# Kernel optimization log

Measured on AMD Instinct MI355X. Metric: run time of the kernel, lower is better.

Reference implementation:

```python
import jax, jax.numpy as jnp
import numpy as np

N, L, K = 2048, 256, 16

def setup_inputs() -> dict:
    rng = np.random.default_rng(0)
    # per level: wavelet index = l (distinct across levels), plus K-1 random distinct rest indices
    sel = np.zeros((L, K), dtype=np.int64)
    wav = np.arange(L, dtype=np.int64)
    all_idx = np.arange(N)
    for l in range(L):
        others = rng.choice(np.delete(all_idx, l), size=K - 1, replace=False)
        sel[l] = np.sort(np.concatenate([[l], others]))
    key = jax.random.key(0)
    k1, k2 = jax.random.split(key)
    M = jax.random.normal(k1, (N, N), dtype=jnp.float32)
    A = 0.5 * (M + M.T)  # symmetric matrix, as MMF expects
    O_all = jax.random.normal(k2, (L, K, K), dtype=jnp.float32) / np.float32(K) ** 0.5
    return {"A": A, "O_all": O_all, "sel_idx": jnp.asarray(sel), "wav_idx": jnp.asarray(wav)}


def reference(A, O_all, sel_idx, wav_idx):
    # Torch builds a dense NxN U = eye with O scattered into the KxK block at
    # sel_idx x sel_idx, then A <- U A U^T and right <- U @ right.
    # Equivalent efficient form: only the K selected rows/cols change.
    n = A.shape[0]

    def step(carry, xs):
        A, right = carry
        O, idx = xs  # O: (K,K), idx: (K,)
        A = A.at[idx].set(O @ A[idx])              # U @ A   : rewrite K rows
        A = A.at[:, idx].set(A[:, idx] @ O.T)      # ... @ U^T: rewrite K cols
        right = right.at[idx].set(O @ right[idx])  # right <- U @ right
        return (A, right), None

    right0 = jnp.eye(n, dtype=A.dtype)
    (A_f, right), _ = jax.lax.scan(step, (A, right0), (O_all, sel_idx))

    # final_active_index: 1 everywhere except wavelet indices
    active = jnp.ones((n,), dtype=A.dtype).at[wav_idx].set(0.0)
    # left_index = eye - diag(diag(outer)) + outer  -> diag all ones, off-diag = a_i*a_j
    left = jnp.outer(active, active)
    left = left.at[jnp.diag_indices(n)].set(1.0)
    D = A_f * left
    A_rec = right.T @ D @ right
    return (A_rec, right, D)
```

## Files before the change

kernel.cpp:

```cpp
#include <hip/hip_runtime.h>

#define N 2048
#define LEV 256
#define KS 16

typedef __attribute__((ext_vector_type(8))) short bfx8;
typedef __attribute__((ext_vector_type(4))) float fx4;
typedef unsigned short u16;
typedef unsigned int u32;

static const size_t NN = (size_t)N * N;

__device__ inline u16 bf16_rne(float f) {
    u32 u = __builtin_bit_cast(u32, f);
    u32 r = (u + 0x7FFFu + ((u >> 16) & 1u)) >> 16;
    return (u16)r;
}
__device__ inline float bf16_f(u16 h) {
    u32 u = ((u32)h) << 16;
    return __builtin_bit_cast(float, u);
}

#define GLDS16(gp, lp) __builtin_amdgcn_global_load_lds( \
    (const __attribute__((address_space(1))) void*)(uintptr_t)(gp), \
    (__attribute__((address_space(3))) void*)(u32)(uintptr_t)(lp), 16, 0, 0)

__device__ inline float qadd(float x) {
#if __has_builtin(__builtin_amdgcn_mov_dpp)
    int a = __builtin_amdgcn_mov_dpp(__builtin_bit_cast(int, x), 0xB1, 0xF, 0xF, true);
    float y = x + __builtin_bit_cast(float, a);
    int b = __builtin_amdgcn_mov_dpp(__builtin_bit_cast(int, y), 0x4E, 0xF, 0xF, true);
    return y + __builtin_bit_cast(float, b);
#else
    float y = x + __shfl_xor(x, 1);
    return y + __shfl_xor(y, 2);
#endif
}

__global__ __launch_bounds__(64)
void front_k(const float* __restrict__ O_all, const int* __restrict__ sel,
             u16* __restrict__ rth,
             const float* __restrict__ A, u16* __restrict__ a2h) {
    __shared__ float x[2048];
    const int lane = threadIdx.x;

    if (blockIdx.x >= 2048) {
        u16* a2l = a2h + NN;
        size_t p = (((size_t)blockIdx.x - 2048) * 64 + lane) * 8;
        float4 v0 = *(const float4*)(A + p);
        float4 v1 = *(const float4*)(A + p + 4);
        float vv[8] = {v0.x, v0.y, v0.z, v0.w, v1.x, v1.y, v1.z, v1.w};
        bfx8 hs, ls;
        #pragma unroll
        for (int i = 0; i < 8; ++i) {
            u16 h = bf16_rne(vv[i]);
            hs[i] = (short)h;
            ls[i] = (short)bf16_rne(vv[i] - bf16_f(h));
        }
        *(bfx8*)(a2h + p) = hs;
        *(bfx8*)(a2l + p) = ls;
        return;
    }

    const int i    = lane >> 2;
    const int kg   = lane & 3;
    const int col  = blockIdx.x;

    const float4 z = make_float4(0.f, 0.f, 0.f, 0.f);
    #pragma unroll
    for (int q = 0; q < 8; ++q) *(float4*)&x[q * 256 + lane * 4] = z;
    if (lane == 0) x[col] = 1.0f;

    const float* obase = O_all + i * KS + kg * 4;
    const int*   gbase = sel + kg * 4;

#define CMP(f, g, wv) { \
    float p = f.x * x[g.x] + f.y * x[g.y] + f.z * x[g.z] + f.w * x[g.w]; \
    p = qadd(p); \
    if (kg == 0) x[wv] = p; }

    float4 f0 = *(const float4*)(obase);
    int4   g0 = *(const int4*)(gbase);
    int    w0 = sel[i];
    float4 f1 = *(const float4*)(obase + 256);
    int4   g1 = *(const int4*)(gbase + KS);
    int    w1 = sel[KS + i];

    for (int l = 0; l < LEV; l += 2) {
        float4 f2, f3; int4 g2, g3; int w2, w3;
        if (l + 2 < LEV) {
            f2 = *(const float4*)(obase + (size_t)(l + 2) * 256);
            g2 = *(const int4*)(gbase + (l + 2) * KS);
            w2 = sel[(l + 2) * KS + i];
            f3 = *(const float4*)(obase + (size_t)(l + 3) * 256);
            g3 = *(const int4*)(gbase + (l + 3) * KS);
            w3 = sel[(l + 3) * KS + i];
        } else { f2 = f0; g2 = g0; w2 = w0; f3 = f1; g3 = g1; w3 = w1; }

        CMP(f0, g0, w0)
        CMP(f1, g1, w1)
        f0 = f2; g0 = g2; w0 = w2;
        f1 = f3; g1 = g3; w1 = w3;
    }
#undef CMP

    u16* rtl = rth + NN;
    #pragma unroll
    for (int q = 0; q < 8; ++q) {
        float4 v = *(const float4*)&x[q * 256 + lane * 4];
        float vv[4] = {v.x, v.y, v.z, v.w};
        u16 hh[4], ll[4];
        #pragma unroll
        for (int e = 0; e < 4; ++e) {
            hh[e] = bf16_rne(vv[e]);
            ll[e] = bf16_rne(vv[e] - bf16_f(hh[e]));
        }
        const size_t po = (size_t)col * N + q * 256 + lane * 4;
        *(ushort4*)(rth + po) = make_ushort4(hh[0], hh[1], hh[2], hh[3]);
        *(ushort4*)(rtl + po) = make_ushort4(ll[0], ll[1], ll[2], ll[3]);
    }
}

__global__ __launch_bounds__(256)
void split_rt_k(const u16* __restrict__ rth, u16* __restrict__ r2h,
                float* __restrict__ Rrm) {
    __shared__ float t[64][65];
    const u16* rtl = rth + NN;
    u16* r2l = r2h + NN;
    const int r0 = (blockIdx.x >> 5) * 64, c0 = (blockIdx.x & 31) * 64;
    #pragma unroll
    for (int i = 0; i < 16; ++i) {
        int q = i * 256 + threadIdx.x;
        int rr = q >> 6, cc = q & 63;
        const size_t po = (size_t)(r0 + rr) * N + c0 + cc;
        t[rr][cc] = bf16_f(rth[po]) + bf16_f(rtl[po]);
    }
    __syncthreads();
    #pragma unroll
    for (int i = 0; i < 16; ++i) {
        int q = i * 256 + threadIdx.x;
        int rr = q >> 6, cc = q & 63;
        float w = t[cc][rr];
        u16 h2 = bf16_rne(w);
        size_t pt = (size_t)(c0 + rr) * N + r0 + cc;
        r2h[pt] = h2;
        r2l[pt] = bf16_rne(w - bf16_f(h2));
        Rrm[pt] = w;
    }
}

__global__ __launch_bounds__(256)
void unsplit_k(const u16* __restrict__ hi, float* __restrict__ dst) {
    const u16* lo = hi + NN;
    size_t p = ((size_t)blockIdx.x * 256 + threadIdx.x) * 8;
    bfx8 hs = *(const bfx8*)(hi + p);
    bfx8 ls = *(const bfx8*)(lo + p);
    float4 o0, o1;
    o0.x = bf16_f((u16)hs[0]) + bf16_f((u16)ls[0]);
    o0.y = bf16_f((u16)hs[1]) + bf16_f((u16)ls[1]);
    o0.z = bf16_f((u16)hs[2]) + bf16_f((u16)ls[2]);
    o0.w = bf16_f((u16)hs[3]) + bf16_f((u16)ls[3]);
    o1.x = bf16_f((u16)hs[4]) + bf16_f((u16)ls[4]);
    o1.y = bf16_f((u16)hs[5]) + bf16_f((u16)ls[5]);
    o1.z = bf16_f((u16)hs[6]) + bf16_f((u16)ls[6]);
    o1.w = bf16_f((u16)hs[7]) + bf16_f((u16)ls[7]);
    *(float4*)(dst + p)     = o0;
    *(float4*)(dst + p + 4) = o1;
}

template<int MASKED, int OMODE>
__global__ __launch_bounds__(256)
void gemm_bf3(const u16* __restrict__ Xp, const u16* __restrict__ Yp,
              float* __restrict__ Cf, u16* __restrict__ Cs,
              const int* __restrict__ wav, int Lw) {
    __shared__ __align__(16) u16 sm[24576];
    __shared__ float rowf[128], colf[64];

    const int tid = threadIdx.x;
    const int xcd = blockIdx.x & 7, idx = blockIdx.x >> 3;
    const int sup = 4 * xcd + (idx >> 4);
    const int wi4 = idx & 15;
    const int by = (sup >> 3) * 4 + (wi4 >> 2);
    const int bx = (sup & 7) * 4 + (wi4 & 3);
    const int i0 = by * 128, j0 = bx * 64;
    const int lane = tid & 63, w = tid >> 6;
    const int wm = (w >> 1) * 64, wn = (w & 1) * 32;
    const int fr = lane & 15;

    if (MASKED) {
        if (tid < 128) rowf[tid] = 1.0f;
        if (tid >= 128 && tid < 192) colf[tid - 128] = 1.0f;
        __syncthreads();
        for (int t = tid; t < Lw; t += 256) {
            int wv = wav[t];
            int dr = wv - i0; if (0 <= dr && dr < 128) rowf[dr] = 0.0f;
            int dc = wv - j0; if (0 <= dc && dc < 64)  colf[dc] = 0.0f;
        }
    }

    fx4 acc[4][2];
    #pragma unroll
    for (int m = 0; m < 4; ++m)
        #pragma unroll
        for (int n = 0; n < 2; ++n)
            acc[m][n] = (fx4)0.0f;

    const u16* Xh = Xp; const u16* Xl = Xp + NN;
    const u16* Yh = Yp; const u16* Yl = Yp + NN;

    const int rl   = lane >> 3;
    const int gcol = ((lane & 7) ^ rl) << 3;
    const int wq   = w * 1024;

    #define STAGE(kt) { \
        const int k0s = (kt) * 64; \
        char* lb0 = (char*)sm + wq; \
        _Pragma("unroll") \
        for (int q = 0; q < 4; ++q) { \
            const int row = q * 32 + w * 8 + rl; \
            const size_t xo = (size_t)(i0 + row) * N + k0s + gcol; \
            GLDS16(Xh + xo, lb0 + q * 4096); \
            GLDS16(Xl + xo, lb0 + 16384 + q * 4096); \
        } \
        _Pragma("unroll") \
        for (int q = 0; q < 2; ++q) { \
            const int row = q * 32 + w * 8 + rl; \
            const size_t yo = (size_t)(j0 + row) * N + k0s + gcol; \
            GLDS16(Yh + yo, lb0 + 32768 + q * 4096); \
            GLDS16(Yl + yo, lb0 + 40960 + q * 4096); \
        } }

    const int kq  = (lane >> 4) << 4;
    const int frx = (fr & 7) << 4;

    #define COMPUTE() { \
        const char* base = (const char*)sm; \
        _Pragma("unroll") \
        for (int s = 0; s < 2; ++s) { \
            const int cb = s * 64 + kq; \
            bfx8 ah[4], al[4]; \
            _Pragma("unroll") \
            for (int m = 0; m < 4; ++m) { \
                const int off = (wm + m * 16 + fr) * 128 + (cb ^ frx); \
                ah[m] = *(const bfx8*)(base + off); \
                al[m] = *(const bfx8*)(base + 16384 + off); \
            } \
            _Pragma("unroll") \
            for (int n = 0; n < 2; ++n) { \
                const int off = (wn + n * 16 + fr) * 128 + (cb ^ frx); \
                bfx8 bh = *(const bfx8*)(base + 32768 + off); \
                bfx8 bl = *(const bfx8*)(base + 40960 + off); \
                _Pragma("unroll") \
                for (int m = 0; m < 4; ++m) { \
                    acc[m][n] = __builtin_amdgcn_mfma_f32_16x16x32_bf16(ah[m], bh, acc[m][n], 0, 0, 0); \
                    acc[m][n] = __builtin_amdgcn_mfma_f32_16x16x32_bf16(ah[m], bl, acc[m][n], 0, 0, 0); \
                    acc[m][n] = __builtin_amdgcn_mfma_f32_16x16x32_bf16(al[m], bh, acc[m][n], 0, 0, 0); \
                } \
            } \
        } }

    constexpr int NT = N / 64;
    for (int kt = 0; kt < NT; ++kt) {
        STAGE(kt)
        __syncthreads();
        COMPUTE()
        __syncthreads();
    }

    const int crow0 = (lane >> 4) * 4;
    #pragma unroll
    for (int m = 0; m < 4; ++m) {
        #pragma unroll
        for (int n = 0; n < 2; ++n) {
            #pragma unroll
            for (int r = 0; r < 4; ++r) {
                const int li = wm + m * 16 + crow0 + r;
                const int lj = wn + n * 16 + fr;
                float v = acc[m][n][r];
                if (MASKED) {
                    if (i0 + li != j0 + lj) v *= rowf[li] * colf[lj];
                }
                const size_t off = (size_t)(i0 + li) * N + j0 + lj;
                if (OMODE == 0) {
                    Cf[off] = v;
                } else {
                    u16 h = bf16_rne(v);
                    Cs[off]      = h;
                    Cs[NN + off] = bf16_rne(v - bf16_f(h));
                }
            }
        }
    }
    #undef STAGE
    #undef COMPUTE
}

template<int MASKED, int OMODE>
__global__ __launch_bounds__(256)
void gemm_sym(const u16* __restrict__ Xp, const u16* __restrict__ Yp,
              float* __restrict__ Cf, u16* __restrict__ Cs,
              const int* __restrict__ wav, int Lw) {
    __shared__ __align__(16) u16 sm[16384];
    __shared__ float rowf[64], colf[64];

    const int tid = threadIdx.x;
    int swz = (blockIdx.x & 7) * 66 + (blockIdx.x >> 3);
    int t = swz, by = 0;
    #pragma unroll 1
    while (t >= 32 - by) { t -= 32 - by; ++by; }
    const int bx = by + t;
    const int i0 = by * 64, j0 = bx * 64;
    const int lane = tid & 63, w = tid >> 6;
    const int wm = (w >> 1) * 32, wn = (w & 1) * 32;
    const int fr = lane & 15;

    if (MASKED) {
        if (tid < 64) rowf[tid] = 1.0f;
        if (tid >= 128 && tid < 192) colf[tid - 128] = 1.0f;
        __syncthreads();
        for (int t2 = tid; t2 < Lw; t2 += 256) {
            int wv = wav[t2];
            int dr = wv - i0; if (0 <= dr && dr < 64) rowf[dr] = 0.0f;
            int dc = wv - j0; if (0 <= dc && dc < 64) colf[dc] = 0.0f;
        }
    }

    fx4 acc[2][2];
    #pragma unroll
    for (int m = 0; m < 2; ++m)
        #pragma unroll
        for (int n = 0; n < 2; ++n)
            acc[m][n] = (fx4)0.0f;

    const u16* Xh = Xp; const u16* Xl = Xp + NN;
    const u16* Yh = Yp; const u16* Yl = Yp + NN;

    const int rl   = lane >> 3;
    const int gcol = ((lane & 7) ^ rl) << 3;
    const int wq   = w * 1024;
    const int kq   = (lane >> 4) << 4;
    const int frx  = (fr & 7) << 4;

    constexpr int NT = N / 64;
    for (int kt = 0; kt < NT; ++kt) {
        const int k0s = kt * 64;
        {
            char* lb0 = (char*)sm + wq;
            #pragma unroll
            for (int q = 0; q < 2; ++q) {
                const int row = q * 32 + w * 8 + rl;
                const size_t xo = (size_t)(i0 + row) * N + k0s + gcol;
                const size_t yo = (size_t)(j0 + row) * N + k0s + gcol;
                GLDS16(Xh + xo, lb0 + q * 4096);
                GLDS16(Xl + xo, lb0 + 8192 + q * 4096);
                GLDS16(Yh + yo, lb0 + 16384 + q * 4096);
                GLDS16(Yl + yo, lb0 + 24576 + q * 4096);
            }
        }
        __syncthreads();
        {
            const char* base = (const char*)sm;
            #pragma unroll
            for (int s = 0; s < 2; ++s) {
                const int cb = s * 64 + kq;
                bfx8 ah[2], al[2];
                #pragma unroll
                for (int m = 0; m < 2; ++m) {
                    const int off = (wm + m * 16 + fr) * 128 + (cb ^ frx);
                    ah[m] = *(const bfx8*)(base + off);
                    al[m] = *(const bfx8*)(base + 8192 + off);
                }
                #pragma unroll
                for (int n = 0; n < 2; ++n) {
                    const int off = (wn + n * 16 + fr) * 128 + (cb ^ frx);
                    bfx8 bh = *(const bfx8*)(base + 16384 + off);
                    bfx8 bl = *(const bfx8*)(base + 24576 + off);
                    #pragma unroll
                    for (int m = 0; m < 2; ++m) {
                        acc[m][n] = __builtin_amdgcn_mfma_f32_16x16x32_bf16(ah[m], bh, acc[m][n], 0, 0, 0);
                        acc[m][n] = __builtin_amdgcn_mfma_f32_16x16x32_bf16(ah[m], bl, acc[m][n], 0, 0, 0);
                        acc[m][n] = __builtin_amdgcn_mfma_f32_16x16x32_bf16(al[m], bh, acc[m][n], 0, 0, 0);
                    }
                }
            }
        }
        __syncthreads();
    }

    float* Ct = (float*)sm;
    const int crow0 = (lane >> 4) * 4;
    #pragma unroll
    for (int m = 0; m < 2; ++m) {
        #pragma unroll
        for (int n = 0; n < 2; ++n) {
            #pragma unroll
            for (int r = 0; r < 4; ++r) {
                const int li = wm + m * 16 + crow0 + r;
                const int lj = wn + n * 16 + fr;
                float v = acc[m][n][r];
                if (MASKED) {
                    if (i0 + li != j0 + lj) v *= rowf[li] * colf[lj];
                }
                Ct[li * 65 + lj] = v;
                const size_t off = (size_t)(i0 + li) * N + j0 + lj;
                if (OMODE == 0) {
                    Cf[off] = v;
                } else {
                    u16 h = bf16_rne(v);
                    Cs[off]      = h;
                    Cs[NN + off] = bf16_rne(v - bf16_f(h));
                }
            }
        }
    }

    if (by != bx) {
        __syncthreads();
        const int rr  = tid >> 2;
        const int cc0 = (tid & 3) * 16;
        float v[16];
        #pragma unroll
        for (int e = 0; e < 16; ++e) v[e] = Ct[(cc0 + e) * 65 + rr];
        const size_t off = (size_t)(j0 + rr) * N + i0 + cc0;
        if (OMODE == 0) {
            #pragma unroll
            for (int q = 0; q < 4; ++q)
                *(float4*)(Cf + off + q * 4) =
                    make_float4(v[q*4], v[q*4+1], v[q*4+2], v[q*4+3]);
        } else {
            bfx8 hs[2], ls[2];
            #pragma unroll
            for (int e = 0; e < 16; ++e) {
                u16 h = bf16_rne(v[e]);
                hs[e >> 3][e & 7] = (short)h;
                ls[e >> 3][e & 7] = (short)bf16_rne(v[e] - bf16_f(h));
            }
            *(bfx8*)(Cs + off)          = hs[0];
            *(bfx8*)(Cs + off + 8)      = hs[1];
            *(bfx8*)(Cs + NN + off)     = ls[0];
            *(bfx8*)(Cs + NN + off + 8) = ls[1];
        }
    }
}

extern "C" void kernel_launch(void* const* d_in, const int* in_sizes, int n_in,
                              void* d_out, int out_size, void* d_ws, size_t ws_size,
                              hipStream_t stream) {
    const float* A     = (const float*)d_in[0];
    const float* O_all = (const float*)d_in[1];
    const int*   sel   = (const int*)d_in[2];
    const int*   wav   = (const int*)d_in[3];
    const int    Lw    = in_sizes[3];

    float* O1 = (float*)d_out;
    float* O2 = O1 + NN;
    float* O3 = O1 + 2 * NN;

    u16*   W1u = (u16*)d_ws;
    u16*   W2u = (u16*)((char*)d_ws + 2 * NN * sizeof(u16));
    u16*   O1u = (u16*)O1;
    u16*   O3u = (u16*)O3;

    const int SGRID = (int)(NN / (256 * 8));

    front_k<<<2048 + (int)(NN / (64 * 8)), 64, 0, stream>>>(O_all, sel, W1u, A, W2u);
    split_rt_k<<<(N / 64) * (N / 64), 256, 0, stream>>>(W1u, O1u, O2);

    gemm_bf3<0, 1><<<512, 256, 0, stream>>>(O1u, W2u, nullptr, O3u, nullptr, 0);
    gemm_sym<1, 1><<<528, 256, 0, stream>>>(O3u, O1u, nullptr, W2u, wav, Lw);
    gemm_bf3<0, 1><<<512, 256, 0, stream>>>(W1u, W2u, nullptr, O3u, nullptr, 0);
    gemm_sym<0, 0><<<528, 256, 0, stream>>>(O3u, W1u, O1, nullptr, nullptr, 0);
    unsplit_k<<<SGRID, 256, 0, stream>>>(W2u, O3);
}
```

Measured before the change: 241.5 us.

## Merge consecutive rotation levels into 32x32 combined operators before the serial sweep

Adds a merge kernel that multiplies each pair of consecutive KxK rotations into one combined operator of up to 32x32 over the union of their index sets. The per-column serial sweep in front_k then runs half as many dependent steps, each a 16-term FMA plus one DPP add instead of a 4-term product plus two DPP adds. This shortens the latency-bound dependency chain of 256 levels. The cost is an extra kernel launch, more global loads per step, and scratch buffers placed in the output region, with padding indices that point into an extended shared array.

```diff
diff --git a/kernel.cpp b/kernel.cpp
--- a/kernel.cpp
+++ b/kernel.cpp
@@ -25,23 +25,70 @@
     (const __attribute__((address_space(1))) void*)(uintptr_t)(gp), \
     (__attribute__((address_space(3))) void*)(u32)(uintptr_t)(lp), 16, 0, 0)
 
-__device__ inline float qadd(float x) {
+__device__ inline float padd1(float x) {
 #if __has_builtin(__builtin_amdgcn_mov_dpp)
     int a = __builtin_amdgcn_mov_dpp(__builtin_bit_cast(int, x), 0xB1, 0xF, 0xF, true);
-    float y = x + __builtin_bit_cast(float, a);
-    int b = __builtin_amdgcn_mov_dpp(__builtin_bit_cast(int, y), 0x4E, 0xF, 0xF, true);
-    return y + __builtin_bit_cast(float, b);
+    return x + __builtin_bit_cast(float, a);
 #else
-    float y = x + __shfl_xor(x, 1);
-    return y + __shfl_xor(y, 2);
+    return x + __shfl_xor(x, 1);
 #endif
 }
 
 __global__ __launch_bounds__(64)
-void front_k(const float* __restrict__ O_all, const int* __restrict__ sel,
+void merge_k(const float* __restrict__ O_all, const int* __restrict__ sel,
+             float* __restrict__ Pg, int* __restrict__ Jg) {
+    __shared__ int Js[32];
+    __shared__ int rowb[32];
+    __shared__ float Ea[32][33], Eb[32][33];
+    const int m = blockIdx.x, lane = threadIdx.x;
+    const int* ia = sel + (2 * m) * KS;
+    const int* ib = sel + (2 * m + 1) * KS;
+
+    if (lane == 0) {
+        int nj = 16;
+        for (int k = 0; k < 16; ++k) Js[k] = ia[k];
+        for (int r = 0; r < 32; ++r) rowb[r] = -1;
+        for (int k = 0; k < 16; ++k) {
+            int v = ib[k], p = -1;
+            for (int t = 0; t < 16; ++t) if (Js[t] == v) p = t;
+            if (p < 0) { p = nj; Js[nj] = v; ++nj; }
+            rowb[p] = k;
+        }
+        for (int r = nj; r < 32; ++r) Js[r] = 2048 + r;
+    }
+    __syncthreads();
+
+    #pragma unroll
+    for (int t = 0; t < 16; ++t) {
+        int e = t * 64 + lane;
+        int r = e >> 5, c = e & 31;
+        float ea = (r < 16) ? (c < 16 ? O_all[(size_t)(2 * m) * 256 + r * 16 + c] : 0.f)
+                            : (r == c ? 1.f : 0.f);
+        int rb = rowb[r], cb = rowb[c];
+        float eb = (rb >= 0) ? (cb >= 0 ? O_all[(size_t)(2 * m + 1) * 256 + rb * 16 + cb] : 0.f)
+                             : (r == c ? 1.f : 0.f);
+        Ea[r][c] = ea;
+        Eb[r][c] = eb;
+    }
+    __syncthreads();
+
+    #pragma unroll
+    for (int t = 0; t < 16; ++t) {
+        int e = t * 64 + lane;
+        int r = e >> 5, c = e & 31;
+        float s = 0.f;
+        #pragma unroll
+        for (int k = 0; k < 32; ++k) s += Eb[r][k] * Ea[k][c];
+        Pg[(size_t)m * 1024 + r * 32 + c] = s;
+    }
+    if (lane < 32) Jg[m * 32 + lane] = Js[lane];
+}
+
+__global__ __launch_bounds__(64)
+void front_k(const float* __restrict__ Pg, const int* __restrict__ Jg,
              u16* __restrict__ rth,
              const float* __restrict__ A, u16* __restrict__ a2h) {
-    __shared__ float x[2048];
+    __shared__ float x[2080];
     const int lane = threadIdx.x;
 
     if (blockIdx.x >= 2048) {
@@ -62,47 +109,63 @@
         return;
     }
 
-    const int i    = lane >> 2;
-    const int kg   = lane & 3;
-    const int col  = blockIdx.x;
-
-    const float4 z = make_float4(0.f, 0.f, 0.f, 0.f);
-    #pragma unroll
-    for (int q = 0; q < 8; ++q) *(float4*)&x[q * 256 + lane * 4] = z;
+    const int r2  = lane >> 1;
+    const int h   = lane & 1;
+    const int col = blockIdx.x;
+
+    for (int v = lane; v < 2080; v += 64) x[v] = 0.0f;
     if (lane == 0) x[col] = 1.0f;
 
-    const float* obase = O_all + i * KS + kg * 4;
-    const int*   gbase = sel + kg * 4;
-
-#define CMP(f, g, wv) { \
-    float p = f.x * x[g.x] + f.y * x[g.y] + f.z * x[g.z] + f.w * x[g.w]; \
-    p = qadd(p); \
-    if (kg == 0) x[wv] = p; }
-
-    float4 f0 = *(const float4*)(obase);
-    int4   g0 = *(const int4*)(gbase);
-    int    w0 = sel[i];
-    float4 f1 = *(const float4*)(obase + 256);
-    int4   g1 = *(const int4*)(gbase + KS);
-    int    w1 = sel[KS + i];
-
-    for (int l = 0; l < LEV; l += 2) {
-        float4 f2, f3; int4 g2, g3; int w2, w3;
-        if (l + 2 < LEV) {
-            f2 = *(const float4*)(obase + (size_t)(l + 2) * 256);
-            g2 = *(const int4*)(gbase + (l + 2) * KS);
-            w2 = sel[(l + 2) * KS + i];
-            f3 = *(const float4*)(obase + (size_t)(l + 3) * 256);
-            g3 = *(const int4*)(gbase + (l + 3) * KS);
-            w3 = sel[(l + 3) * KS + i];
-        } else { f2 = f0; g2 = g0; w2 = w0; f3 = f1; g3 = g1; w3 = w1; }
-
-        CMP(f0, g0, w0)
-        CMP(f1, g1, w1)
-        f0 = f2; g0 = g2; w0 = w2;
-        f1 = f3; g1 = g3; w1 = w3;
-    }
-#undef CMP
+    #define LOADPJ(m_, P0,P1,P2,P3, J0,J1,J2,J3, JW) { \
+        const float* pb = Pg + (size_t)(m_) * 1024 + r2 * 32 + h * 16; \
+        P0 = *(const float4*)(pb);      P1 = *(const float4*)(pb + 4); \
+        P2 = *(const float4*)(pb + 8);  P3 = *(const float4*)(pb + 12); \
+        const int* jb = Jg + (m_) * 32; \
+        J0 = *(const int4*)(jb + h * 16);      J1 = *(const int4*)(jb + h * 16 + 4); \
+        J2 = *(const int4*)(jb + h * 16 + 8);  J3 = *(const int4*)(jb + h * 16 + 12); \
+        JW = jb[r2]; }
+
+    float4 cP0, cP1, cP2, cP3, nP0, nP1, nP2, nP3, tP0, tP1, tP2, tP3;
+    int4   cJ0, cJ1, cJ2, cJ3, nJ0, nJ1, nJ2, nJ3, tJ0, tJ1, tJ2, tJ3;
+    int    cjw, njw, tjw;
+
+    LOADPJ(0, cP0,cP1,cP2,cP3, cJ0,cJ1,cJ2,cJ3, cjw)
+    LOADPJ(1, nP0,nP1,nP2,nP3, nJ0,nJ1,nJ2,nJ3, njw)
+
+    for (int m = 0; m < LEV / 2; ++m) {
+        if (m + 2 < LEV / 2) {
+            LOADPJ(m + 2, tP0,tP1,tP2,tP3, tJ0,tJ1,tJ2,tJ3, tjw)
+        } else {
+            tP0 = nP0; tP1 = nP1; tP2 = nP2; tP3 = nP3;
+            tJ0 = nJ0; tJ1 = nJ1; tJ2 = nJ2; tJ3 = nJ3; tjw = njw;
+        }
+
+        float p = 0.f;
+        p = fmaf(cP0.x, x[cJ0.x], p);
+        p = fmaf(cP0.y, x[cJ0.y], p);
+        p = fmaf(cP0.z, x[cJ0.z], p);
+        p = fmaf(cP0.w, x[cJ0.w], p);
+        p = fmaf(cP1.x, x[cJ1.x], p);
+        p = fmaf(cP1.y, x[cJ1.y], p);
+        p = fmaf(cP1.z, x[cJ1.z], p);
+        p = fmaf(cP1.w, x[cJ1.w], p);
+        p = fmaf(cP2.x, x[cJ2.x], p);
+        p = fmaf(cP2.y, x[cJ2.y], p);
+        p = fmaf(cP2.z, x[cJ2.z], p);
+        p = fmaf(cP2.w, x[cJ2.w], p);
+        p = fmaf(cP3.x, x[cJ3.x], p);
+        p = fmaf(cP3.y, x[cJ3.y], p);
+        p = fmaf(cP3.z, x[cJ3.z], p);
+        p = fmaf(cP3.w, x[cJ3.w], p);
+        p = padd1(p);
+        if (h == 0) x[cjw] = p;
+
+        cP0 = nP0; cP1 = nP1; cP2 = nP2; cP3 = nP3;
+        cJ0 = nJ0; cJ1 = nJ1; cJ2 = nJ2; cJ3 = nJ3; cjw = njw;
+        nP0 = tP0; nP1 = tP1; nP2 = tP2; nP3 = tP3;
+        nJ0 = tJ0; nJ1 = tJ1; nJ2 = tJ2; nJ3 = tJ3; njw = tjw;
+    }
+    #undef LOADPJ
 
     u16* rtl = rth + NN;
     #pragma unroll
@@ -461,9 +524,13 @@
     u16*   O1u = (u16*)O1;
     u16*   O3u = (u16*)O3;
 
+    float* Pg = O1;
+    int*   Jg = (int*)(O1 + 131072);
+
     const int SGRID = (int)(NN / (256 * 8));
 
-    front_k<<<2048 + (int)(NN / (64 * 8)), 64, 0, stream>>>(O_all, sel, W1u, A, W2u);
+    merge_k<<<LEV / 2, 64, 0, stream>>>(O_all, sel, Pg, Jg);
+    front_k<<<2048 + (int)(NN / (64 * 8)), 64, 0, stream>>>(Pg, Jg, W1u, A, W2u);
     split_rt_k<<<(N / 64) * (N / 64), 256, 0, stream>>>(W1u, O1u, O2);
 
     gemm_bf3<0, 1><<<512, 256, 0, stream>>>(O1u, W2u, nullptr, O3u, nullptr, 0);
```

New measurement: 308.6 us. 1.28x slower.
